# Kernel optimization log

Hardware: AMD Instinct MI355X
Metric: run time of the kernel (lower is better)

Reference implementation:

```python
import jax, jax.numpy as jnp
import numpy as np

B, S, D, H = 4, 2048, 1024, 16
HD = D // H
NEG = -1000000.0  # matches sequence_mask fill value in the torch source


def setup_inputs() -> dict:
    key = jax.random.key(0)
    kq, kk, kv, kl, k1, k2, k3, k4 = jax.random.split(key, 8)
    scale = 1.0 / np.sqrt(D)
    return {
        "queries": jax.random.normal(kq, (B, S, D), dtype=jnp.float32),
        "keys": jax.random.normal(kk, (B, S, D), dtype=jnp.float32),
        "values": jax.random.normal(kv, (B, S, D), dtype=jnp.float32),
        "valid_lens": jax.random.randint(kl, (B,), 0, S, dtype=jnp.int64),
        "Wq": jax.random.normal(k1, (D, D), dtype=jnp.float32) * scale,
        "Wk": jax.random.normal(k2, (D, D), dtype=jnp.float32) * scale,
        "Wv": jax.random.normal(k3, (D, D), dtype=jnp.float32) * scale,
        "Wo": jax.random.normal(k4, (D, D), dtype=jnp.float32) * scale,
    }


def reference(queries, keys, values, valid_lens, Wq, Wk, Wv, Wo):
    def split_heads(x):  # [B,S,D] -> [B,H,S,HD]
        return x.reshape(B, S, H, HD).transpose(0, 2, 1, 3)

    q = split_heads(queries @ Wq)
    k = split_heads(keys @ Wk)
    v = split_heads(values @ Wv)

    scores = jnp.einsum("bhqd,bhkd->bhqk", q, k) / np.sqrt(HD)
    # padding mask over key positions: key index < valid_len[b]
    key_mask = jnp.arange(S)[None, :] < valid_lens[:, None]  # [B,S]
    scores = jnp.where(key_mask[:, None, None, :], scores, NEG)
    attn = jax.nn.softmax(scores, axis=-1)
    # dropout p=0.0 -> identity
    out = jnp.einsum("bhqk,bhkd->bhqd", attn, v)
    out = out.transpose(0, 2, 1, 3).reshape(B, S, D)  # merge heads
    return out @ Wo
```

## Files before the change

kernel.cpp:

```cpp
#include <hip/hip_runtime.h>
#include <hip/hip_bf16.h>

#define B_ 4
#define S_ 2048
#define D_ 1024
#define H_ 16
#define HD_ 64
#define M_ 8192
#define NEGV -1000000.0f
#define CEXP 0.18033688011112042f

typedef __attribute__((ext_vector_type(8))) __bf16 bf16x8;
typedef __attribute__((ext_vector_type(4))) float f32x4;
typedef __attribute__((ext_vector_type(16))) float f32x16;

__device__ __forceinline__ f32x4 mfma16(bf16x8 a, bf16x8 b, f32x4 c) {
  return __builtin_amdgcn_mfma_f32_16x16x32_bf16(a, b, c, 0, 0, 0);
}
__device__ __forceinline__ f32x16 mfma32(bf16x8 a, bf16x8 b, f32x16 c) {
  return __builtin_amdgcn_mfma_f32_32x32x16_bf16(a, b, c, 0, 0, 0);
}

#if __has_builtin(__builtin_amdgcn_exp2f)
__device__ __forceinline__ float exp2_hw(float x) { return __builtin_amdgcn_exp2f(x); }
#else
__device__ __forceinline__ float exp2_hw(float x) {
  float r;
  asm volatile("v_exp_f32 %0, %1" : "=v"(r) : "v"(x));
  return r;
}
#endif

__device__ __forceinline__ unsigned bf16rz(float x) {
  unsigned u = __float_as_uint(x);
  return (u + 0x7FFFu + ((u >> 16) & 1u)) >> 16;
}
__device__ __forceinline__ unsigned pk2bf(float a, float b) {
  unsigned ua = __float_as_uint(a), ub = __float_as_uint(b);
  ua = ua + 0x7FFFu + ((ua >> 16) & 1u);
  ub = ub + 0x7FFFu + ((ub >> 16) & 1u);
  return (ua >> 16) | (ub & 0xFFFF0000u);
}

__device__ __forceinline__ void gld_lds16(const __hip_bfloat16* g, __hip_bfloat16* l) {
  __builtin_amdgcn_global_load_lds(
      (const __attribute__((address_space(1))) void*)g,
      (__attribute__((address_space(3))) void*)l, 16, 0, 0);
}

__global__ __launch_bounds__(256) void convert_x3(const float* __restrict__ Xq,
                                                  const float* __restrict__ Xk,
                                                  const float* __restrict__ Xv,
                                                  __hip_bfloat16* __restrict__ Yq,
                                                  __hip_bfloat16* __restrict__ Yk,
                                                  __hip_bfloat16* __restrict__ Yv,
                                                  int n4, const int* __restrict__ vl) {
  const int z = blockIdx.y;
  const float* X = (z == 0) ? Xq : (z == 1) ? Xk : Xv;
  __hip_bfloat16* Y = (z == 0) ? Yq : (z == 1) ? Yk : Yv;
  int i = blockIdx.x * blockDim.x + threadIdx.x;
  if (i >= n4) return;
  if (z) {
    int gm = i >> 8;
    int vlen = vl[gm >> 11];
    if (vlen > 0 && (gm & 2047) >= ((vlen + 63) & ~63)) return;
  }
  float4 v = reinterpret_cast<const float4*>(X)[i];
  uint2 o;
  o.x = pk2bf(v.x, v.y);
  o.y = pk2bf(v.z, v.w);
  reinterpret_cast<uint2*>(Y)[i] = o;
}

__global__ __launch_bounds__(256) void convert_wt4(const float* __restrict__ W0,
                                                   const float* __restrict__ W1,
                                                   const float* __restrict__ W2,
                                                   const float* __restrict__ W3,
                                                   __hip_bfloat16* __restrict__ WtBase) {
  const int z = blockIdx.z;
  const float* W = (z == 0) ? W0 : (z == 1) ? W1 : (z == 2) ? W2 : W3;
  __hip_bfloat16* Wt = WtBase + (size_t)z * D_ * D_;
  __shared__ float tile[32][33];
  int c0 = blockIdx.x * 32, r0 = blockIdx.y * 32;
  int tx = threadIdx.x, ty = threadIdx.y;
#pragma unroll
  for (int rr = ty; rr < 32; rr += 8)
    tile[rr][tx] = W[(size_t)(r0 + rr) * D_ + c0 + tx];
  __syncthreads();
#pragma unroll
  for (int rr = ty; rr < 32; rr += 8)
    reinterpret_cast<unsigned short*>(Wt)[(size_t)(c0 + rr) * D_ + r0 + tx] =
        (unsigned short)bf16rz(tile[tx][rr]);
}

template <int EPI>
__global__ __launch_bounds__(256) void gemm_bt(const __hip_bfloat16* __restrict__ A,
                                               const __hip_bfloat16* __restrict__ Bt,
                                               void* __restrict__ Cout,
                                               const int* __restrict__ vskip,
                                               float cscale) {
  int id = blockIdx.y * gridDim.x + blockIdx.x;
  int cpx = (gridDim.x * gridDim.y) >> 3;
  int nid = (id & 7) * cpx + (id >> 3);
  const int m0 = (nid >> 3) * 128, n0 = (nid & 7) * 128;
  if (vskip) {
    int vlen = vskip[m0 >> 11];
    if (vlen > 0 && (m0 & 2047) >= ((vlen + 63) & ~63)) return;
  }
  const int t = threadIdx.x, lane = t & 63, wid = t >> 6;
  const int lc = lane & 15, g = lane >> 4;
  const int srow8 = lane >> 3, sg8 = lane & 7;
  __shared__ __align__(16) __hip_bfloat16 smem[2][2][128 * 64];
  f32x4 acc[4][4] = {};
  const int wm = (wid & 1) * 64, wn = (wid >> 1) * 64;

  auto stage = [&](int buf, int k0) {
#pragma unroll
    for (int c = 0; c < 4; ++c) {
      int ci = c * 4 + wid;
      int row = ci * 8 + srow8;
      int sg = sg8 ^ (row & 7);
      gld_lds16(A + (size_t)(m0 + row) * D_ + k0 + sg * 8, &smem[buf][0][ci * 512]);
      gld_lds16(Bt + (size_t)(n0 + row) * D_ + k0 + sg * 8, &smem[buf][1][ci * 512]);
    }
  };

  stage(0, 0);
  asm volatile("s_waitcnt vmcnt(0)" ::: "memory");
  __syncthreads();
  int cur = 0;

  for (int kt = 0; kt < D_ / 64; ++kt) {
    if (kt + 1 < D_ / 64) stage(cur ^ 1, (kt + 1) * 64);
    const __hip_bfloat16* As = smem[cur][0];
    const __hip_bfloat16* Bs = smem[cur][1];
#pragma unroll
    for (int kh = 0; kh < 2; ++kh) {
      bf16x8 af[4], bf[4];
#pragma unroll
      for (int mi = 0; mi < 4; ++mi) {
        int r = wm + mi * 16 + lc;
        af[mi] = *reinterpret_cast<const bf16x8*>(
            As + r * 64 + (((kh * 4 + g) ^ (r & 7)) << 3));
        int rn = wn + mi * 16 + lc;
        bf[mi] = *reinterpret_cast<const bf16x8*>(
            Bs + rn * 64 + (((kh * 4 + g) ^ (rn & 7)) << 3));
      }
#pragma unroll
      for (int mi = 0; mi < 4; ++mi)
#pragma unroll
        for (int ni = 0; ni < 4; ++ni)
          acc[mi][ni] = mfma16(af[mi], bf[ni], acc[mi][ni]);
    }
    asm volatile("s_waitcnt vmcnt(0)" ::: "memory");
    __syncthreads();
    cur ^= 1;
  }

#pragma unroll
  for (int mi = 0; mi < 4; ++mi) {
#pragma unroll
    for (int ni = 0; ni < 4; ++ni) {
#pragma unroll
      for (int i = 0; i < 4; ++i) {
        int gm = m0 + wm + mi * 16 + g * 4 + i;
        int gn = n0 + wn + ni * 16 + lc;
        float val = acc[mi][ni][i] * cscale;
        if constexpr (EPI == 0) {
          int b = gm >> 11, s = gm & 2047, h = gn >> 6, d = gn & 63;
          reinterpret_cast<unsigned short*>(
              Cout)[(((size_t)(b * H_ + h) * S_ + s) << 6) + d] =
              (unsigned short)bf16rz(val);
        } else if constexpr (EPI == 1) {
          int b = gm >> 11, s = gm & 2047, h = gn >> 6, d = gn & 63;
          reinterpret_cast<unsigned short*>(
              Cout)[(((size_t)(b * H_ + h) * HD_ + d) << 11) + s] =
              (unsigned short)bf16rz(val);
        } else {
          ((float*)Cout)[(size_t)gm * D_ + gn] = val;
        }
      }
    }
  }
}

__global__ __launch_bounds__(512) void attn(const __hip_bfloat16* __restrict__ Qh,
                                            const __hip_bfloat16* __restrict__ Kh,
                                            const __hip_bfloat16* __restrict__ Vt,
                                            const int* __restrict__ vlens,
                                            __hip_bfloat16* __restrict__ O,
                                            int* __restrict__ ctr) {
  const int t = threadIdx.x, lane = t & 63, w = t >> 6;
  const int wq = w & 3, up = w >> 2;
  const int q = lane & 31;
  const int hh = lane >> 5;

  int va = vlens[0], vb = vlens[1], vc = vlens[2], vd = vlens[3];
  int ia = 0, ib = 1, ic = 2, id_ = 3;
  {
    int tv, ti;
#define CSWAP(x, xi, y, yi) \
    if (y > x) { tv = x; x = y; y = tv; ti = xi; xi = yi; yi = ti; }
    CSWAP(va, ia, vb, ib) CSWAP(vc, ic, vd, id_)
    CSWAP(va, ia, vc, ic) CSWAP(vb, ib, vd, id_)
    CSWAP(vb, ib, vc, ic)
#undef CSWAP
  }
  __shared__ int s_unit;
  __shared__ __align__(16) __hip_bfloat16 smem[3][8192];

  while (true) {
    if (t == 0) s_unit = atomicAdd(ctr, 1);
    __syncthreads();
    const int u = s_unit;
    if (u >= 512) break;
    const int rank = u >> 7;
    const int b = (rank == 0) ? ia : (rank == 1) ? ib : (rank == 2) ? ic : id_;
    const int vlen = (rank == 0) ? va : (rank == 1) ? vb : (rank == 2) ? vc : vd;
    const int r = u & 127;
    const int h = r & 15, qtp = r >> 4;
    const int bh = b * 16 + h;

    const __hip_bfloat16* Qb = Qh + (size_t)bh * S_ * HD_;
    const __hip_bfloat16* Kb = Kh + (size_t)bh * S_ * HD_;
    const __hip_bfloat16* Vb = Vt + (size_t)bh * HD_ * S_;

    const int qrow = qtp * 256 + up * 128 + wq * 32 + q;
    bf16x8 qf[4];
#pragma unroll
    for (int kk = 0; kk < 4; ++kk)
      qf[kk] = *reinterpret_cast<const bf16x8*>(Qb + (size_t)qrow * HD_ + kk * 16 + hh * 8);

    f32x16 accT[2] = {};
    float l_half = 0.f;

    const int srow = lane >> 3;
    const int sg = lane & 7;
    const float maskv = (vlen == 0) ? 0.f : NEGV;
    const int kv_end = (vlen == 0) ? S_ : min(S_, (vlen + 63) & ~63);
    const int nt = kv_end >> 6;

    auto stage = [&](int buf, int tile) {
      int kv = tile * 64;
      int rr = w * 8 + srow;
      int gs = sg ^ (rr & 7);
      gld_lds16(Kb + (size_t)(kv + rr) * HD_ + gs * 8, smem[buf] + (w * 8) * 64);
      gld_lds16(Vb + (size_t)rr * S_ + kv + gs * 8, smem[buf] + 4096 + (w * 8) * 64);
    };

    stage(0, 0);
    if (nt > 1) stage(1, 1);
    int bc = 0;
    int bs = (nt > 2) ? 2 : 0;

    for (int tt = 0; tt < nt; ++tt) {
      if (tt + 1 < nt) {
        asm volatile("s_waitcnt vmcnt(2)" ::: "memory");
      } else {
        asm volatile("s_waitcnt vmcnt(0)" ::: "memory");
      }
      __syncthreads();
      if (tt + 2 < nt) stage(bs, tt + 2);

      const __hip_bfloat16* Ks = smem[bc];
      const __hip_bfloat16* Vs = smem[bc] + 4096;

      f32x16 sc[2];
#pragma unroll
      for (int ct = 0; ct < 2; ++ct) {
        f32x16 a = {};
#pragma unroll
        for (int kk = 0; kk < 4; ++kk) {
          int row = ct * 32 + q;
          bf16x8 kf = *reinterpret_cast<const bf16x8*>(
              Ks + row * 64 + (((kk * 2 + hh) ^ (row & 7)) << 3));
          a = mfma32(kf, qf[kk], a);
        }
        sc[ct] = a;
      }

      int kv = tt * 64;
      if (kv + 64 > vlen) {
#pragma unroll
        for (int ct = 0; ct < 2; ++ct)
#pragma unroll
          for (int rr = 0; rr < 16; ++rr) {
            int j = kv + ct * 32 + (rr & 3) + 8 * (rr >> 2) + 4 * hh;
            if (j >= vlen) sc[ct][rr] = maskv;
          }
      }

      uint wlo[8], whi[8];
      float rs = 0.f;
#pragma unroll
      for (int a2 = 0; a2 < 8; ++a2) {
        float p0 = exp2_hw(sc[a2 >> 2][(a2 & 3) * 4 + 0]);
        float p1 = exp2_hw(sc[a2 >> 2][(a2 & 3) * 4 + 1]);
        float p2 = exp2_hw(sc[a2 >> 2][(a2 & 3) * 4 + 2]);
        float p3 = exp2_hw(sc[a2 >> 2][(a2 & 3) * 4 + 3]);
        rs += (p0 + p1) + (p2 + p3);
        wlo[a2] = pk2bf(p0, p1);
        whi[a2] = pk2bf(p2, p3);
      }
      l_half += rs;

#pragma unroll
      for (int kk = 0; kk < 4; ++kk) {
        uint glo = wlo[2 * kk], ghi = whi[2 * kk];
        uint flo = wlo[2 * kk + 1], fhi = whi[2 * kk + 1];
        uint slo = hh ? glo : flo, shi = hh ? ghi : fhi;
        uint rlo = __shfl_xor(slo, 32), rhi = __shfl_xor(shi, 32);
        union { uint u[4]; bf16x8 v; } pf;
        pf.u[0] = hh ? rlo : glo;
        pf.u[1] = hh ? rhi : ghi;
        pf.u[2] = hh ? flo : rlo;
        pf.u[3] = hh ? fhi : rhi;
#pragma unroll
        for (int ctd = 0; ctd < 2; ++ctd) {
          int vr = ctd * 32 + q;
          bf16x8 vf = *reinterpret_cast<const bf16x8*>(
              Vs + vr * 64 + (((kk * 2 + hh) ^ (vr & 7)) << 3));
          accT[ctd] = mfma32(vf, pf.v, accT[ctd]);
        }
      }
      bc = (bc == 2) ? 0 : bc + 1;
      bs = (bs == 2) ? 0 : bs + 1;
    }
    __syncthreads();

    float l_tot = l_half + __shfl_xor(l_half, 32);
    float inv = 1.f / l_tot;
    __hip_bfloat16* Ot = smem[0] + w * 2048;
#pragma unroll
    for (int ctd = 0; ctd < 2; ++ctd)
#pragma unroll
      for (int a2 = 0; a2 < 4; ++a2) {
        uint2 o;
        o.x = pk2bf(accT[ctd][a2 * 4 + 0] * inv, accT[ctd][a2 * 4 + 1] * inv);
        o.y = pk2bf(accT[ctd][a2 * 4 + 2] * inv, accT[ctd][a2 * 4 + 3] * inv);
        int gs8 = (ctd * 8 + a2 * 2 + hh) ^ ((q & 7) << 1);
        *reinterpret_cast<uint2*>(Ot + q * 64 + gs8 * 4) = o;
      }
#pragma unroll
    for (int rr = 0; rr < 4; ++rr) {
      int row = rr * 8 + (lane >> 3);
      int c16 = lane & 7;
      float4 v4 = *reinterpret_cast<const float4*>(
          Ot + row * 64 + (((c16 * 2) ^ ((row & 7) << 1)) << 2));
      int s = qtp * 256 + up * 128 + wq * 32 + row;
      *reinterpret_cast<float4*>(O + ((size_t)b * S_ + s) * D_ + h * HD_ + c16 * 8) = v4;
    }
  }
}

extern "C" void kernel_launch(void* const* d_in, const int* in_sizes, int n_in,
                              void* d_out, int out_size, void* d_ws, size_t ws_size,
                              hipStream_t stream) {
  const float* Xq = (const float*)d_in[0];
  const float* Xk = (const float*)d_in[1];
  const float* Xv = (const float*)d_in[2];
  const int* vl = (const int*)d_in[3];
  const float* Wq = (const float*)d_in[4];
  const float* Wk = (const float*)d_in[5];
  const float* Wv = (const float*)d_in[6];
  const float* Wo = (const float*)d_in[7];
  float* out = (float*)d_out;

  char* ws = (char*)d_ws;
  const size_t XB = (size_t)M_ * D_ * 2;
  const size_t WB = (size_t)D_ * D_ * 2;
  __hip_bfloat16* xq = (__hip_bfloat16*)(ws);
  __hip_bfloat16* xk = (__hip_bfloat16*)(ws + XB);
  __hip_bfloat16* xv = (__hip_bfloat16*)(ws + 2 * XB);
  __hip_bfloat16* wtq = (__hip_bfloat16*)(ws + 3 * XB);
  __hip_bfloat16* wtk = (__hip_bfloat16*)(ws + 3 * XB + WB);
  __hip_bfloat16* wtv = (__hip_bfloat16*)(ws + 3 * XB + 2 * WB);
  __hip_bfloat16* wto = (__hip_bfloat16*)(ws + 3 * XB + 3 * WB);
  __hip_bfloat16* Qh = (__hip_bfloat16*)(ws + 3 * XB + 4 * WB);
  __hip_bfloat16* Kh = (__hip_bfloat16*)(ws + 4 * XB + 4 * WB);
  __hip_bfloat16* Vh = (__hip_bfloat16*)(ws + 5 * XB + 4 * WB);
  __hip_bfloat16* Obuf = xq;
  int* ctr = (int*)xk;

  convert_wt4<<<dim3(32, 32, 4), dim3(32, 8), 0, stream>>>(Wq, Wk, Wv, Wo, wtq);

  const int n4 = M_ * D_ / 4;
  convert_x3<<<dim3(n4 / 256, 3), 256, 0, stream>>>(Xq, Xk, Xv, xq, xk, xv, n4, vl);

  dim3 gg(M_ / 128, D_ / 128);
  gemm_bt<0><<<gg, 256, 0, stream>>>(xq, wtq, Qh, nullptr, CEXP);
  gemm_bt<0><<<gg, 256, 0, stream>>>(xk, wtk, Kh, vl, 1.0f);
  gemm_bt<1><<<gg, 256, 0, stream>>>(xv, wtv, Vh, vl, 1.0f);

  hipMemsetAsync(ctr, 0, sizeof(int), stream);
  attn<<<dim3(512), 512, 0, stream>>>(Qh, Kh, Vh, vl, Obuf, ctr);
  gemm_bt<2><<<gg, 256, 0, stream>>>(Obuf, wto, out, nullptr, 1.0f);
}
```

Before: 200.5 us.

## Batch Q/K/V projections into one launch and raise wave priority around attention MFMAs

Adds a gemm_qkv kernel that computes the three projection GEMMs as one grid with a z dimension, replacing three separate gemm_bt launches. This fills the GPU with more concurrent blocks and removes tail effects between launches, while keeping the valid-length skip for K and V. The attention inner loop also gets s_setprio raised around the QK and PV MFMA sections, so matrix work is issued preferentially over other waves' softmax. The new GEMM duplicates the old body, with a double-buffered loop that waits for all loads each iteration, so its pipelining may differ from the original gemm_bt.

```diff
diff --git a/kernel.cpp b/kernel.cpp
--- a/kernel.cpp
+++ b/kernel.cpp
@@ -91,6 +91,103 @@
   for (int rr = ty; rr < 32; rr += 8)
     reinterpret_cast<unsigned short*>(Wt)[(size_t)(c0 + rr) * D_ + r0 + tx] =
         (unsigned short)bf16rz(tile[tx][rr]);
+}
+
+__global__ __launch_bounds__(256) void gemm_qkv(const __hip_bfloat16* __restrict__ Aq,
+                                                const __hip_bfloat16* __restrict__ Ak,
+                                                const __hip_bfloat16* __restrict__ Av,
+                                                const __hip_bfloat16* __restrict__ WtBase,
+                                                __hip_bfloat16* __restrict__ Qh,
+                                                __hip_bfloat16* __restrict__ Kh,
+                                                __hip_bfloat16* __restrict__ Vh,
+                                                const int* __restrict__ vl) {
+  const int z = blockIdx.z;
+  const __hip_bfloat16* A = (z == 0) ? Aq : (z == 1) ? Ak : Av;
+  const __hip_bfloat16* Bt = WtBase + (size_t)z * D_ * D_;
+  __hip_bfloat16* Cout = (z == 0) ? Qh : (z == 1) ? Kh : Vh;
+  const float cscale = (z == 0) ? CEXP : 1.0f;
+  const int epi = (z == 2) ? 1 : 0;
+
+  int id = blockIdx.y * gridDim.x + blockIdx.x;
+  int cpx = (gridDim.x * gridDim.y) >> 3;
+  int nid = (id & 7) * cpx + (id >> 3);
+  const int m0 = (nid >> 3) * 128, n0 = (nid & 7) * 128;
+  if (z) {
+    int vlen = vl[m0 >> 11];
+    if (vlen > 0 && (m0 & 2047) >= ((vlen + 63) & ~63)) return;
+  }
+  const int t = threadIdx.x, lane = t & 63, wid = t >> 6;
+  const int lc = lane & 15, g = lane >> 4;
+  const int srow8 = lane >> 3, sg8 = lane & 7;
+  __shared__ __align__(16) __hip_bfloat16 smem[2][2][128 * 64];
+  f32x4 acc[4][4] = {};
+  const int wm = (wid & 1) * 64, wn = (wid >> 1) * 64;
+
+  auto stage = [&](int buf, int k0) {
+#pragma unroll
+    for (int c = 0; c < 4; ++c) {
+      int ci = c * 4 + wid;
+      int row = ci * 8 + srow8;
+      int sg = sg8 ^ (row & 7);
+      gld_lds16(A + (size_t)(m0 + row) * D_ + k0 + sg * 8, &smem[buf][0][ci * 512]);
+      gld_lds16(Bt + (size_t)(n0 + row) * D_ + k0 + sg * 8, &smem[buf][1][ci * 512]);
+    }
+  };
+
+  stage(0, 0);
+  asm volatile("s_waitcnt vmcnt(0)" ::: "memory");
+  __syncthreads();
+  int cur = 0;
+
+  for (int kt = 0; kt < D_ / 64; ++kt) {
+    if (kt + 1 < D_ / 64) stage(cur ^ 1, (kt + 1) * 64);
+    const __hip_bfloat16* As = smem[cur][0];
+    const __hip_bfloat16* Bs = smem[cur][1];
+#pragma unroll
+    for (int kh = 0; kh < 2; ++kh) {
+      bf16x8 af[4], bf[4];
+#pragma unroll
+      for (int mi = 0; mi < 4; ++mi) {
+        int r = wm + mi * 16 + lc;
+        af[mi] = *reinterpret_cast<const bf16x8*>(
+            As + r * 64 + (((kh * 4 + g) ^ (r & 7)) << 3));
+        int rn = wn + mi * 16 + lc;
+        bf[mi] = *reinterpret_cast<const bf16x8*>(
+            Bs + rn * 64 + (((kh * 4 + g) ^ (rn & 7)) << 3));
+      }
+#pragma unroll
+      for (int mi = 0; mi < 4; ++mi)
+#pragma unroll
+        for (int ni = 0; ni < 4; ++ni)
+          acc[mi][ni] = mfma16(af[mi], bf[ni], acc[mi][ni]);
+    }
+    asm volatile("s_waitcnt vmcnt(0)" ::: "memory");
+    __syncthreads();
+    cur ^= 1;
+  }
+
+#pragma unroll
+  for (int mi = 0; mi < 4; ++mi) {
+#pragma unroll
+    for (int ni = 0; ni < 4; ++ni) {
+#pragma unroll
+      for (int i = 0; i < 4; ++i) {
+        int gm = m0 + wm + mi * 16 + g * 4 + i;
+        int gn = n0 + wn + ni * 16 + lc;
+        float val = acc[mi][ni][i] * cscale;
+        int b = gm >> 11, s = gm & 2047, h = gn >> 6, d = gn & 63;
+        if (epi == 0) {
+          reinterpret_cast<unsigned short*>(
+              Cout)[(((size_t)(b * H_ + h) * S_ + s) << 6) + d] =
+              (unsigned short)bf16rz(val);
+        } else {
+          reinterpret_cast<unsigned short*>(
+              Cout)[(((size_t)(b * H_ + h) * HD_ + d) << 11) + s] =
+              (unsigned short)bf16rz(val);
+        }
+      }
+    }
+  }
 }
 
 template <int EPI>
@@ -266,6 +363,7 @@
       const __hip_bfloat16* Vs = smem[bc] + 4096;
 
       f32x16 sc[2];
+      __builtin_amdgcn_s_setprio(1);
 #pragma unroll
       for (int ct = 0; ct < 2; ++ct) {
         f32x16 a = {};
@@ -278,6 +376,7 @@
         }
         sc[ct] = a;
       }
+      __builtin_amdgcn_s_setprio(0);
 
       int kv = tt * 64;
       if (kv + 64 > vlen) {
@@ -304,6 +403,7 @@
       }
       l_half += rs;
 
+      __builtin_amdgcn_s_setprio(1);
 #pragma unroll
       for (int kk = 0; kk < 4; ++kk) {
         uint glo = wlo[2 * kk], ghi = whi[2 * kk];
@@ -323,6 +423,7 @@
           accT[ctd] = mfma32(vf, pf.v, accT[ctd]);
         }
       }
+      __builtin_amdgcn_s_setprio(0);
       bc = (bc == 2) ? 0 : bc + 1;
       bs = (bs == 2) ? 0 : bs + 1;
     }
@@ -373,8 +474,6 @@
   __hip_bfloat16* xk = (__hip_bfloat16*)(ws + XB);
   __hip_bfloat16* xv = (__hip_bfloat16*)(ws + 2 * XB);
   __hip_bfloat16* wtq = (__hip_bfloat16*)(ws + 3 * XB);
-  __hip_bfloat16* wtk = (__hip_bfloat16*)(ws + 3 * XB + WB);
-  __hip_bfloat16* wtv = (__hip_bfloat16*)(ws + 3 * XB + 2 * WB);
   __hip_bfloat16* wto = (__hip_bfloat16*)(ws + 3 * XB + 3 * WB);
   __hip_bfloat16* Qh = (__hip_bfloat16*)(ws + 3 * XB + 4 * WB);
   __hip_bfloat16* Kh = (__hip_bfloat16*)(ws + 4 * XB + 4 * WB);
@@ -387,12 +486,10 @@
   const int n4 = M_ * D_ / 4;
   convert_x3<<<dim3(n4 / 256, 3), 256, 0, stream>>>(Xq, Xk, Xv, xq, xk, xv, n4, vl);
 
-  dim3 gg(M_ / 128, D_ / 128);
-  gemm_bt<0><<<gg, 256, 0, stream>>>(xq, wtq, Qh, nullptr, CEXP);
-  gemm_bt<0><<<gg, 256, 0, stream>>>(xk, wtk, Kh, vl, 1.0f);
-  gemm_bt<1><<<gg, 256, 0, stream>>>(xv, wtv, Vh, vl, 1.0f);
+  gemm_qkv<<<dim3(M_ / 128, D_ / 128, 3), 256, 0, stream>>>(xq, xk, xv, wtq,
+                                                            Qh, Kh, Vh, vl);
 
   hipMemsetAsync(ctr, 0, sizeof(int), stream);
   attn<<<dim3(512), 512, 0, stream>>>(Qh, Kh, Vh, vl, Obuf, ctr);
-  gemm_bt<2><<<gg, 256, 0, stream>>>(Obuf, wto, out, nullptr, 1.0f);
-}
+  gemm_bt<2><<<dim3(M_ / 128, D_ / 128), 256, 0, stream>>>(Obuf, wto, out, nullptr, 1.0f);
+}
```

New measurement: 205.7 us. 1.03x slower.

## Stage KV tiles in pairs with double buffering to halve barriers

Applied to the files above, without the earlier changes.

Replaces the three-buffer, one-tile-per-step LDS pipeline with two buffers that each hold two 64-row K/V tiles. Each loop step prefetches the next pair while computing the current two tiles, so there is one wait and one barrier per two tiles instead of one per tile. The trade-off is a shallower prefetch window, since the load is issued only one step ahead and then fully drained, and LDS use rises from 48KB to 64KB, which may lower occupancy.

```diff
diff --git a/kernel.cpp b/kernel.cpp
--- a/kernel.cpp
+++ b/kernel.cpp
@@ -207,7 +207,7 @@
 #undef CSWAP
   }
   __shared__ int s_unit;
-  __shared__ __align__(16) __hip_bfloat16 smem[3][8192];
+  __shared__ __align__(16) __hip_bfloat16 smem[2][16384];
 
   while (true) {
     if (t == 0) s_unit = atomicAdd(ctr, 1);
@@ -239,94 +239,102 @@
     const float maskv = (vlen == 0) ? 0.f : NEGV;
     const int kv_end = (vlen == 0) ? S_ : min(S_, (vlen + 63) & ~63);
     const int nt = kv_end >> 6;
-
-    auto stage = [&](int buf, int tile) {
-      int kv = tile * 64;
+    const int npair = (nt + 1) >> 1;
+
+    auto stagePair = [&](int buf, int pt) {
       int rr = w * 8 + srow;
       int gs = sg ^ (rr & 7);
-      gld_lds16(Kb + (size_t)(kv + rr) * HD_ + gs * 8, smem[buf] + (w * 8) * 64);
-      gld_lds16(Vb + (size_t)rr * S_ + kv + gs * 8, smem[buf] + 4096 + (w * 8) * 64);
+#pragma unroll
+      for (int half = 0; half < 2; ++half) {
+        int tile = 2 * pt + half;
+        if (tile >= nt) break;
+        int kv = tile * 64;
+        gld_lds16(Kb + (size_t)(kv + rr) * HD_ + gs * 8,
+                  smem[buf] + half * 8192 + (w * 8) * 64);
+        gld_lds16(Vb + (size_t)rr * S_ + kv + gs * 8,
+                  smem[buf] + half * 8192 + 4096 + (w * 8) * 64);
+      }
     };
 
-    stage(0, 0);
-    if (nt > 1) stage(1, 1);
-    int bc = 0;
-    int bs = (nt > 2) ? 2 : 0;
-
-    for (int tt = 0; tt < nt; ++tt) {
-      if (tt + 1 < nt) {
-        asm volatile("s_waitcnt vmcnt(2)" ::: "memory");
-      } else {
-        asm volatile("s_waitcnt vmcnt(0)" ::: "memory");
-      }
-      __syncthreads();
-      if (tt + 2 < nt) stage(bs, tt + 2);
-
-      const __hip_bfloat16* Ks = smem[bc];
-      const __hip_bfloat16* Vs = smem[bc] + 4096;
-
-      f32x16 sc[2];
-#pragma unroll
-      for (int ct = 0; ct < 2; ++ct) {
-        f32x16 a = {};
+    stagePair(0, 0);
+    asm volatile("s_waitcnt vmcnt(0)" ::: "memory");
+    __syncthreads();
+    int cur = 0;
+
+    for (int p = 0; p < npair; ++p) {
+      if (p + 1 < npair) stagePair(cur ^ 1, p + 1);
+
+#pragma unroll
+      for (int half = 0; half < 2; ++half) {
+        int tile = 2 * p + half;
+        if (tile >= nt) break;
+        const __hip_bfloat16* Ks = smem[cur] + half * 8192;
+        const __hip_bfloat16* Vs = Ks + 4096;
+
+        f32x16 sc[2];
+#pragma unroll
+        for (int ct = 0; ct < 2; ++ct) {
+          f32x16 a = {};
+#pragma unroll
+          for (int kk = 0; kk < 4; ++kk) {
+            int row = ct * 32 + q;
+            bf16x8 kf = *reinterpret_cast<const bf16x8*>(
+                Ks + row * 64 + (((kk * 2 + hh) ^ (row & 7)) << 3));
+            a = mfma32(kf, qf[kk], a);
+          }
+          sc[ct] = a;
+        }
+
+        int kv = tile * 64;
+        if (kv + 64 > vlen) {
+#pragma unroll
+          for (int ct = 0; ct < 2; ++ct)
+#pragma unroll
+            for (int rr = 0; rr < 16; ++rr) {
+              int j = kv + ct * 32 + (rr & 3) + 8 * (rr >> 2) + 4 * hh;
+              if (j >= vlen) sc[ct][rr] = maskv;
+            }
+        }
+
+        uint wlo[8], whi[8];
+        float rs = 0.f;
+#pragma unroll
+        for (int a2 = 0; a2 < 8; ++a2) {
+          float p0 = exp2_hw(sc[a2 >> 2][(a2 & 3) * 4 + 0]);
+          float p1 = exp2_hw(sc[a2 >> 2][(a2 & 3) * 4 + 1]);
+          float p2 = exp2_hw(sc[a2 >> 2][(a2 & 3) * 4 + 2]);
+          float p3 = exp2_hw(sc[a2 >> 2][(a2 & 3) * 4 + 3]);
+          rs += (p0 + p1) + (p2 + p3);
+          wlo[a2] = pk2bf(p0, p1);
+          whi[a2] = pk2bf(p2, p3);
+        }
+        l_half += rs;
+
 #pragma unroll
         for (int kk = 0; kk < 4; ++kk) {
-          int row = ct * 32 + q;
-          bf16x8 kf = *reinterpret_cast<const bf16x8*>(
-              Ks + row * 64 + (((kk * 2 + hh) ^ (row & 7)) << 3));
-          a = mfma32(kf, qf[kk], a);
-        }
-        sc[ct] = a;
-      }
-
-      int kv = tt * 64;
-      if (kv + 64 > vlen) {
-#pragma unroll
-        for (int ct = 0; ct < 2; ++ct)
-#pragma unroll
-          for (int rr = 0; rr < 16; ++rr) {
-            int j = kv + ct * 32 + (rr & 3) + 8 * (rr >> 2) + 4 * hh;
-            if (j >= vlen) sc[ct][rr] = maskv;
+          uint glo = wlo[2 * kk], ghi = whi[2 * kk];
+          uint flo = wlo[2 * kk + 1], fhi = whi[2 * kk + 1];
+          uint slo = hh ? glo : flo, shi = hh ? ghi : fhi;
+          uint rlo = __shfl_xor(slo, 32), rhi = __shfl_xor(shi, 32);
+          union { uint u[4]; bf16x8 v; } pf;
+          pf.u[0] = hh ? rlo : glo;
+          pf.u[1] = hh ? rhi : ghi;
+          pf.u[2] = hh ? flo : rlo;
+          pf.u[3] = hh ? fhi : rhi;
+#pragma unroll
+          for (int ctd = 0; ctd < 2; ++ctd) {
+            int vr = ctd * 32 + q;
+            bf16x8 vf = *reinterpret_cast<const bf16x8*>(
+                Vs + vr * 64 + (((kk * 2 + hh) ^ (vr & 7)) << 3));
+            accT[ctd] = mfma32(vf, pf.v, accT[ctd]);
           }
-      }
-
-      uint wlo[8], whi[8];
-      float rs = 0.f;
-#pragma unroll
-      for (int a2 = 0; a2 < 8; ++a2) {
-        float p0 = exp2_hw(sc[a2 >> 2][(a2 & 3) * 4 + 0]);
-        float p1 = exp2_hw(sc[a2 >> 2][(a2 & 3) * 4 + 1]);
-        float p2 = exp2_hw(sc[a2 >> 2][(a2 & 3) * 4 + 2]);
-        float p3 = exp2_hw(sc[a2 >> 2][(a2 & 3) * 4 + 3]);
-        rs += (p0 + p1) + (p2 + p3);
-        wlo[a2] = pk2bf(p0, p1);
-        whi[a2] = pk2bf(p2, p3);
-      }
-      l_half += rs;
-
-#pragma unroll
-      for (int kk = 0; kk < 4; ++kk) {
-        uint glo = wlo[2 * kk], ghi = whi[2 * kk];
-        uint flo = wlo[2 * kk + 1], fhi = whi[2 * kk + 1];
-        uint slo = hh ? glo : flo, shi = hh ? ghi : fhi;
-        uint rlo = __shfl_xor(slo, 32), rhi = __shfl_xor(shi, 32);
-        union { uint u[4]; bf16x8 v; } pf;
-        pf.u[0] = hh ? rlo : glo;
-        pf.u[1] = hh ? rhi : ghi;
-        pf.u[2] = hh ? flo : rlo;
-        pf.u[3] = hh ? fhi : rhi;
-#pragma unroll
-        for (int ctd = 0; ctd < 2; ++ctd) {
-          int vr = ctd * 32 + q;
-          bf16x8 vf = *reinterpret_cast<const bf16x8*>(
-              Vs + vr * 64 + (((kk * 2 + hh) ^ (vr & 7)) << 3));
-          accT[ctd] = mfma32(vf, pf.v, accT[ctd]);
         }
       }
-      bc = (bc == 2) ? 0 : bc + 1;
-      bs = (bs == 2) ? 0 : bs + 1;
+
+      asm volatile("s_waitcnt vmcnt(0)" ::: "memory");
+      __syncthreads();
+      cur ^= 1;
     }
-    __syncthreads();
 
     float l_tot = l_half + __shfl_xor(l_half, 32);
     float inv = 1.f / l_tot;
```

After: 194.7 us. -2.9%, faster.
